# Kernel tuning notes

Hardware: AMD Instinct MI355X
Metric: run time of the kernel (lower is better)

## Reference

```python
import jax, jax.numpy as jnp
import numpy as np

D = 32       # d_model / hidden_size
H = 4        # n_heads
E = D // H   # head dim = 8
N = 2000     # nodes (hardcoded in FourierBlock weights / proj_class)
L = 96       # seq_len
MODES = (1, 4, 5)  # self.index hardcoded in FourierBlock
KAVG = 25    # moving_avg kernel (first of kernel list; layer uses res[0], trends[0])


def setup_inputs() -> dict:
    key = jax.random.key(0)
    ks = jax.random.split(key, 12)
    B = 8
    x = jax.random.normal(ks[0], (B, N, L, D), jnp.float32)
    lin = lambda k: jax.random.normal(k, (D, D), jnp.float32) * (1.0 / np.sqrt(D))
    scale = 1.0 / (D * D)  # FourierBlock: scale * torch.rand(...)
    W1 = jax.random.uniform(ks[5], (N, H, E, E, len(MODES)), jnp.float32) * scale
    W2 = jax.random.uniform(ks[6], (N, H, E, E, len(MODES)), jnp.float32) * scale
    return {
        "x": x,
        "Wq": lin(ks[1]), "bq": jnp.zeros((D,), jnp.float32),
        "Wk": lin(ks[2]), "bk": jnp.zeros((D,), jnp.float32),
        "Wv": lin(ks[3]), "bv": jnp.zeros((D,), jnp.float32),
        "Wo": lin(ks[4]), "bo": jnp.zeros((D,), jnp.float32),
        "W1": W1, "W2": W2,
    }


def _fourier_block(q, W1, W2):
    # q: [B, N, L, H, E] -> permute to [B, N, H, E, L] (torch: x = q.permute(0,1,3,4,2))
    B, Nn, Ll, Hh, Ee = q.shape
    xq = jnp.transpose(q, (0, 1, 3, 4, 2))
    x_ft = jnp.fft.rfft(xq, axis=-1)                 # [B, N, H, E, L//2+1] complex
    idx = jnp.array(MODES)
    xm = x_ft[..., idx]                              # [B, N, H, E, M]
    Wc = W1 + 1j * W2                                # complex per-node frequency weights
    out_m = jnp.einsum('bnhem,nheom->bnhom', xm, Wc.astype(jnp.complex64))
    F = Ll // 2 + 1
    out_ft = jnp.zeros((B, Nn, Hh, Ee, F), jnp.complex64).at[..., idx].set(out_m)
    y = jnp.fft.irfft(out_ft, n=Ll, axis=-1)         # [B, N, H, E, L]
    return jnp.transpose(y, (0, 1, 4, 2, 3))         # [B, N, L, H, E]


def _moving_avg(x, k):
    # replicate-pad the time axis by (k-1)//2 on each side, then mean over window k (stride 1)
    pad = (k - 1) // 2
    xp = jnp.pad(x, ((0, 0), (0, 0), (pad, pad), (0, 0)), mode='edge')
    cs = jnp.cumsum(xp, axis=2)
    cs = jnp.concatenate([jnp.zeros_like(cs[:, :, :1]), cs], axis=2)
    return (cs[:, :, k:] - cs[:, :, :-k]) / k        # [B, N, T, C]


def reference(x, Wq, bq, Wk, bk, Wv, bv, Wo, bo, W1, W2):
    B, Nn, Ll, Dm = x.shape
    # AutoCorrelationLayer projections
    q = (x @ Wq.T + bq).reshape(B, Nn, Ll, H, E)
    k = (x @ Wk.T + bk).reshape(B, Nn, Ll, H, E)   # faithful: computed, unused by FourierBlock
    v = (x @ Wv.T + bv).reshape(B, Nn, Ll, H, E)   # faithful: computed, unused by FourierBlock
    out = _fourier_block(q, W1, W2)                 # inner_correlation(q, k, v)
    out = out.reshape(B, Nn, Ll, Dm)
    new_x = out @ Wo.T + bo                         # out_projection
    # FFTDecompLayer: residual + series decomposition (eval mode, dropout=0)
    xr = x + new_x
    trend = _moving_avg(xr, KAVG)
    res = xr - trend
    return res
```

## Files before the change

### kernel.cpp

```cpp
#include <hip/hip_runtime.h>


#define N_NODES 2000

__global__ __launch_bounds__(256, 4)
void fused_fourier_decomp(const float* __restrict__ x,
                          const float* __restrict__ Wq,
                          const float* __restrict__ Wo,
                          const float* __restrict__ bo,
                          const float* __restrict__ W1,
                          const float* __restrict__ W2,
                          float* __restrict__ out)
{
  __shared__ __align__(16) float xT[32 * 97];
  __shared__ __align__(16) float basis[96 * 8];
  __shared__ __align__(16) float Wq_s[32 * 33];
  __shared__ __align__(16) float Wo_s[32 * 33];
  __shared__ __align__(16) float W1_s[768];
  __shared__ __align__(16) float W2_s[768];
  __shared__ __align__(16) float Z_s[32 * 8];
  __shared__ float bo_s[32];
  float* const pp = xT;
  float* const sbuf = xT + 1600;

  const int t = threadIdx.x;
  const int bid = blockIdx.x;
  const int n = bid % N_NODES;
  const size_t base = (size_t)bid * (96 * 32);

  const int d = t & 31;
  const int g = t >> 5;
  const int l0 = g * 12;

  float xv[12];
#pragma unroll
  for (int i = 0; i < 12; ++i)
    xv[i] = x[base + (size_t)(l0 + i) * 32 + d];

  for (int i = t; i < 1024; i += 256) {
    Wq_s[(i >> 5) * 33 + (i & 31)] = Wq[i];
    Wo_s[(i >> 5) * 33 + (i & 31)] = Wo[i];
  }
  {
    const float* W1p = W1 + n * 768;
    const float* W2p = W2 + n * 768;
    for (int i = t; i < 768; i += 256) {
      W1_s[i] = W1p[i];
      W2_s[i] = W2p[i];
    }
  }
  if (t < 32) bo_s[t] = bo[t];

  if (t < 96) {
    const int modes[3] = {1, 4, 5};
#pragma unroll
    for (int m = 0; m < 3; ++m) {
      int r = (modes[m] * t) % 96;
      float ang = (float)r * (6.28318530717958647692f / 96.0f);
      float sv, cv;
      sincosf(ang, &sv, &cv);
      basis[t * 8 + m] = cv;
      basis[t * 8 + 3 + m] = sv;
    }
    basis[t * 8 + 6] = 0.0f;
    basis[t * 8 + 7] = 0.0f;
  }
  __syncthreads();

  {
    float a0 = 0.f, a1 = 0.f, a2 = 0.f, a3 = 0.f, a4 = 0.f, a5 = 0.f;
#pragma unroll
    for (int i = 0; i < 12; ++i) {
      const int l = l0 + i;
      const float4 b0 = *(const float4*)&basis[l * 8];
      const float2 b1 = *(const float2*)&basis[l * 8 + 4];
      const float v = xv[i];
      a0 = fmaf(v, b0.x, a0);
      a1 = fmaf(v, b0.y, a1);
      a2 = fmaf(v, b0.z, a2);
      a3 = fmaf(v, b0.w, a3);
      a4 = fmaf(v, b1.x, a4);
      a5 = fmaf(v, b1.y, a5);
    }
    pp[g * 192 + 0 * 32 + d] = a0;
    pp[g * 192 + 1 * 32 + d] = a1;
    pp[g * 192 + 2 * 32 + d] = a2;
    pp[g * 192 + 3 * 32 + d] = a3;
    pp[g * 192 + 4 * 32 + d] = a4;
    pp[g * 192 + 5 * 32 + d] = a5;
  }
  __syncthreads();

  if (t < 64) {
    const int c = t & 31;
    const int jj = t >> 5;
    float* const csb = sbuf;
    float* const xsb = sbuf + 256;
    float* const osb = sbuf;

#pragma unroll
    for (int k = 0; k < 3; ++k) {
      const int j = jj * 3 + k;
      float s = 0.f;
#pragma unroll
      for (int gg = 0; gg < 8; ++gg) s += pp[gg * 192 + j * 32 + c];
      csb[c * 8 + j] = s;
    }
    __builtin_amdgcn_wave_barrier();

    {
      float X0 = 0.f, X1 = 0.f, X2 = 0.f;
#pragma unroll
      for (int dd = 0; dd < 32; ++dd) {
        const float w = Wq_s[c * 33 + dd];
        const int cb = dd * 8 + jj * 3;
        X0 = fmaf(w, csb[cb + 0], X0);
        X1 = fmaf(w, csb[cb + 1], X1);
        X2 = fmaf(w, csb[cb + 2], X2);
      }
      const float sgn = jj ? -1.f : 1.f;
      xsb[c * 8 + jj * 3 + 0] = sgn * X0;
      xsb[c * 8 + jj * 3 + 1] = sgn * X1;
      xsb[c * 8 + jj * 3 + 2] = sgn * X2;
    }
    __builtin_amdgcn_wave_barrier();

    {
      const int h = (t >> 3) & 3;
      const int o = t & 7;
      float od0 = 0.f, od1 = 0.f, od2 = 0.f;
#pragma unroll
      for (int e = 0; e < 8; ++e) {
        const int cp = h * 8 + e;
        const float4 xa = *(const float4*)&xsb[cp * 8];
        const float2 xb = *(const float2*)&xsb[cp * 8 + 4];
        const int wi = (cp * 8 + o) * 3;
        {
          const float w1 = W1_s[wi + 0], w2 = W2_s[wi + 0];
          const float a = jj ? w1 : -w2;
          const float b = jj ? w2 : w1;
          od0 = fmaf(xa.x, b, fmaf(xa.w, a, od0));
        }
        {
          const float w1 = W1_s[wi + 1], w2 = W2_s[wi + 1];
          const float a = jj ? w1 : -w2;
          const float b = jj ? w2 : w1;
          od1 = fmaf(xa.y, b, fmaf(xb.x, a, od1));
        }
        {
          const float w1 = W1_s[wi + 2], w2 = W2_s[wi + 2];
          const float a = jj ? w1 : -w2;
          const float b = jj ? w2 : w1;
          od2 = fmaf(xa.z, b, fmaf(xb.y, a, od2));
        }
      }
      const int cp = h * 8 + o;
      osb[cp * 8 + jj * 3 + 0] = od0;
      osb[cp * 8 + jj * 3 + 1] = od1;
      osb[cp * 8 + jj * 3 + 2] = od2;
    }
    __builtin_amdgcn_wave_barrier();

    {
      float z0 = 0.f, z1 = 0.f, z2 = 0.f;
#pragma unroll
      for (int cc = 0; cc < 32; ++cc) {
        const float w = Wo_s[c * 33 + cc];
        const int ob = cc * 8 + jj * 3;
        z0 = fmaf(w, osb[ob + 0], z0);
        z1 = fmaf(w, osb[ob + 1], z1);
        z2 = fmaf(w, osb[ob + 2], z2);
      }
      Z_s[c * 8 + jj * 3 + 0] = z0;
      Z_s[c * 8 + jj * 3 + 1] = z1;
      Z_s[c * 8 + jj * 3 + 2] = z2;
    }
  }
  __syncthreads();

  float xr[12];
  {
    const float4 z0 = *(const float4*)&Z_s[d * 8];
    const float2 z1 = *(const float2*)&Z_s[d * 8 + 4];
    const float bov = bo_s[d];
#pragma unroll
    for (int i = 0; i < 12; ++i) {
      const int l = l0 + i;
      const float4 b0 = *(const float4*)&basis[l * 8];
      const float2 b1 = *(const float2*)&basis[l * 8 + 4];
      const float v = z0.x * b0.x + z0.y * b0.y + z0.z * b0.z
                    - z0.w * b0.w - z1.x * b1.x - z1.y * b1.y;
      const float r = fmaf(v, (1.0f / 48.0f), bov) + xv[i];
      xr[i] = r;
      xT[d * 97 + l] = r;
    }
  }
  __syncthreads();

  {
    const float* col = &xT[d * 97];
    float lowv[12];
    float S = 0.f;
#pragma unroll
    for (int j = 0; j < 12; ++j) {
      int idx = l0 - 12 + j;
      idx = idx < 0 ? 0 : idx;
      lowv[j] = col[idx];
      S += lowv[j];
    }
#pragma unroll
    for (int i = 0; i < 12; ++i) S += xr[i];
    {
      int idx = l0 + 12;
      idx = idx > 95 ? 95 : idx;
      S += col[idx];
    }
#pragma unroll
    for (int i = 0; i < 12; ++i) {
      const int l = l0 + i;
      const float res = xr[i] - S * (1.0f / 25.0f);
      out[base + (size_t)l * 32 + d] = res;
      int hi = l + 13;
      hi = hi > 95 ? 95 : hi;
      S += col[hi] - lowv[i];
    }
  }
}

extern "C" void kernel_launch(void* const* d_in, const int* in_sizes, int n_in,
                              void* d_out, int out_size, void* d_ws, size_t ws_size,
                              hipStream_t stream) {
  (void)n_in; (void)out_size; (void)d_ws; (void)ws_size;
  const float* x  = (const float*)d_in[0];
  const float* Wq = (const float*)d_in[1];
  const float* Wo = (const float*)d_in[7];
  const float* bo = (const float*)d_in[8];
  const float* W1 = (const float*)d_in[9];
  const float* W2 = (const float*)d_in[10];
  float* out = (float*)d_out;

  const int blocks = in_sizes[0] / (96 * 32);
  fused_fourier_decomp<<<blocks, 256, 0, stream>>>(x, Wq, Wo, bo, W1, W2, out);
}
```

Measured before the change: 396.6 us.

## Process two same-node tiles per 512-thread block to share weight setup

Each block now handles two (batch, node) tiles that share the same node, using 512 threads. The per-block setup is loaded once and shared by both tiles: the Wq/Wo matrices, the per-node W1/W2 Fourier weights and the basis table. The per-node weights are aliased into the unused tail of the shared buffer to keep LDS usage down. The aim is to halve redundant setup traffic and shared-memory fills. It relies on half the tile count being a multiple of the node count (true for B=8), and the tighter launch bounds (512 threads, 8 blocks) may force register limits.

```diff
diff --git a/kernel.cpp b/kernel.cpp
--- a/kernel.cpp
+++ b/kernel.cpp
@@ -3,33 +3,39 @@
 
 #define N_NODES 2000
 
-__global__ __launch_bounds__(256, 4)
+__global__ __launch_bounds__(512, 8)
 void fused_fourier_decomp(const float* __restrict__ x,
                           const float* __restrict__ Wq,
                           const float* __restrict__ Wo,
                           const float* __restrict__ bo,
                           const float* __restrict__ W1,
                           const float* __restrict__ W2,
-                          float* __restrict__ out)
+                          float* __restrict__ out,
+                          const int halfTiles)
 {
-  __shared__ __align__(16) float xT[32 * 97];
+  __shared__ __align__(16) float xT[2 * 32 * 97];
   __shared__ __align__(16) float basis[96 * 8];
   __shared__ __align__(16) float Wq_s[32 * 33];
   __shared__ __align__(16) float Wo_s[32 * 33];
-  __shared__ __align__(16) float W1_s[768];
-  __shared__ __align__(16) float W2_s[768];
-  __shared__ __align__(16) float Z_s[32 * 8];
+  __shared__ __align__(16) float Z_s[2 * 32 * 8];
   __shared__ float bo_s[32];
-  float* const pp = xT;
-  float* const sbuf = xT + 1600;
-
-  const int t = threadIdx.x;
-  const int bid = blockIdx.x;
-  const int n = bid % N_NODES;
-  const size_t base = (size_t)bid * (96 * 32);
-
-  const int d = t & 31;
-  const int g = t >> 5;
+
+  const int t    = threadIdx.x;
+  const int tile = t >> 8;
+  const int tt   = t & 255;
+  const int n    = blockIdx.x % N_NODES;
+  const size_t bid  = (size_t)blockIdx.x + (size_t)tile * (size_t)halfTiles;
+  const size_t base = bid * (96 * 32);
+
+  float* const xTt  = xT + tile * 3104;
+  float* const pp   = xTt;
+  float* const sbuf = xTt + 1600;
+  float* const W1_s = xT + 2112;
+  float* const W2_s = xT + 3104 + 2112;
+  float* const Zt   = Z_s + tile * 256;
+
+  const int d  = tt & 31;
+  const int g  = tt >> 5;
   const int l0 = g * 12;
 
   float xv[12];
@@ -37,14 +43,14 @@
   for (int i = 0; i < 12; ++i)
     xv[i] = x[base + (size_t)(l0 + i) * 32 + d];
 
-  for (int i = t; i < 1024; i += 256) {
+  for (int i = t; i < 1024; i += 512) {
     Wq_s[(i >> 5) * 33 + (i & 31)] = Wq[i];
     Wo_s[(i >> 5) * 33 + (i & 31)] = Wo[i];
   }
   {
     const float* W1p = W1 + n * 768;
     const float* W2p = W2 + n * 768;
-    for (int i = t; i < 768; i += 256) {
+    for (int i = t; i < 768; i += 512) {
       W1_s[i] = W1p[i];
       W2_s[i] = W2p[i];
     }
@@ -91,9 +97,9 @@
   }
   __syncthreads();
 
-  if (t < 64) {
-    const int c = t & 31;
-    const int jj = t >> 5;
+  if (tt < 64) {
+    const int c  = tt & 31;
+    const int jj = tt >> 5;
     float* const csb = sbuf;
     float* const xsb = sbuf + 256;
     float* const osb = sbuf;
@@ -126,8 +132,8 @@
     __builtin_amdgcn_wave_barrier();
 
     {
-      const int h = (t >> 3) & 3;
-      const int o = t & 7;
+      const int h = (tt >> 3) & 3;
+      const int o = tt & 7;
       float od0 = 0.f, od1 = 0.f, od2 = 0.f;
 #pragma unroll
       for (int e = 0; e < 8; ++e) {
@@ -171,17 +177,17 @@
         z1 = fmaf(w, osb[ob + 1], z1);
         z2 = fmaf(w, osb[ob + 2], z2);
       }
-      Z_s[c * 8 + jj * 3 + 0] = z0;
-      Z_s[c * 8 + jj * 3 + 1] = z1;
-      Z_s[c * 8 + jj * 3 + 2] = z2;
+      Zt[c * 8 + jj * 3 + 0] = z0;
+      Zt[c * 8 + jj * 3 + 1] = z1;
+      Zt[c * 8 + jj * 3 + 2] = z2;
     }
   }
   __syncthreads();
 
   float xr[12];
   {
-    const float4 z0 = *(const float4*)&Z_s[d * 8];
-    const float2 z1 = *(const float2*)&Z_s[d * 8 + 4];
+    const float4 z0 = *(const float4*)&Zt[d * 8];
+    const float2 z1 = *(const float2*)&Zt[d * 8 + 4];
     const float bov = bo_s[d];
 #pragma unroll
     for (int i = 0; i < 12; ++i) {
@@ -192,13 +198,13 @@
                     - z0.w * b0.w - z1.x * b1.x - z1.y * b1.y;
       const float r = fmaf(v, (1.0f / 48.0f), bov) + xv[i];
       xr[i] = r;
-      xT[d * 97 + l] = r;
-    }
-  }
-  __syncthreads();
-
-  {
-    const float* col = &xT[d * 97];
+      xTt[d * 97 + l] = r;
+    }
+  }
+  __syncthreads();
+
+  {
+    const float* col = &xTt[d * 97];
     float lowv[12];
     float S = 0.f;
 #pragma unroll
@@ -239,6 +245,8 @@
   const float* W2 = (const float*)d_in[10];
   float* out = (float*)d_out;
 
-  const int blocks = in_sizes[0] / (96 * 32);
-  fused_fourier_decomp<<<blocks, 256, 0, stream>>>(x, Wq, Wo, bo, W1, W2, out);
+  const int tiles = in_sizes[0] / (96 * 32);
+  const int halfTiles = tiles / 2;
+  fused_fourier_decomp<<<halfTiles, 512, 0, stream>>>(x, Wq, Wo, bo, W1, W2, out,
+                                                      halfTiles);
 }
```

New measurement: 434.8 us. 9.6% more time.

## Drop Wq/Wo shared staging and repack spectral weights for vectorized LDS reads

Applied to the files above, without the earlier changes.

Wq and Wo are no longer staged in shared memory. Each thread reads its row straight from global into registers as float4. W1 and W2 are interleaved into one padded per-output-channel shared array, so the complex mode mix can read them with float4/float2 loads. The intermediate csb/xsb/osb buffers are transposed to mode-major order so the projections and reductions use vector LDS accesses. This cuts shared-memory footprint and LDS instruction count, but adds global (cache) loads in the 64-thread section and a scattered-index write when staging W1/W2.

```diff
diff --git a/kernel.cpp b/kernel.cpp
--- a/kernel.cpp
+++ b/kernel.cpp
@@ -14,14 +14,13 @@
 {
   __shared__ __align__(16) float xT[32 * 97];
   __shared__ __align__(16) float basis[96 * 8];
-  __shared__ __align__(16) float Wq_s[32 * 33];
-  __shared__ __align__(16) float Wo_s[32 * 33];
-  __shared__ __align__(16) float W1_s[768];
-  __shared__ __align__(16) float W2_s[768];
+  __shared__ __align__(16) float W12_s[32 * 68];
   __shared__ __align__(16) float Z_s[32 * 8];
   __shared__ float bo_s[32];
-  float* const pp = xT;
-  float* const sbuf = xT + 1600;
+  float* const pp  = xT;
+  float* const csb = xT + 1600;
+  float* const xsb = xT + 1792;
+  float* const osb = xT + 1600;
 
   const int t = threadIdx.x;
   const int bid = blockIdx.x;
@@ -37,16 +36,17 @@
   for (int i = 0; i < 12; ++i)
     xv[i] = x[base + (size_t)(l0 + i) * 32 + d];
 
-  for (int i = t; i < 1024; i += 256) {
-    Wq_s[(i >> 5) * 33 + (i & 31)] = Wq[i];
-    Wo_s[(i >> 5) * 33 + (i & 31)] = Wo[i];
-  }
-  {
-    const float* W1p = W1 + n * 768;
-    const float* W2p = W2 + n * 768;
+  {
+    const float* W1p = W1 + (size_t)n * 768;
+    const float* W2p = W2 + (size_t)n * 768;
     for (int i = t; i < 768; i += 256) {
-      W1_s[i] = W1p[i];
-      W2_s[i] = W2p[i];
+      const int m = i % 3;
+      const int o = (i / 3) & 7;
+      const int e = (i / 24) & 7;
+      const int h = i / 192;
+      const int dst = (h * 8 + o) * 68 + e * 8 + m;
+      W12_s[dst]     = W1p[i];
+      W12_s[dst + 3] = W2p[i];
     }
   }
   if (t < 32) bo_s[t] = bo[t];
@@ -92,88 +92,115 @@
   __syncthreads();
 
   if (t < 64) {
-    const int c = t & 31;
+    const int c  = t & 31;
     const int jj = t >> 5;
-    float* const csb = sbuf;
-    float* const xsb = sbuf + 256;
-    float* const osb = sbuf;
-
-#pragma unroll
-    for (int k = 0; k < 3; ++k) {
-      const int j = jj * 3 + k;
-      float s = 0.f;
-#pragma unroll
-      for (int gg = 0; gg < 8; ++gg) s += pp[gg * 192 + j * 32 + c];
-      csb[c * 8 + j] = s;
+
+    if (t < 48) {
+      const int j = t >> 3, cq = t & 7;
+      float4 acc = make_float4(0.f, 0.f, 0.f, 0.f);
+#pragma unroll
+      for (int gg = 0; gg < 8; ++gg) {
+        const float4 p = *(const float4*)&pp[gg * 192 + j * 32 + cq * 4];
+        acc.x += p.x; acc.y += p.y; acc.z += p.z; acc.w += p.w;
+      }
+      *(float4*)&csb[j * 32 + cq * 4] = acc;
     }
     __builtin_amdgcn_wave_barrier();
 
     {
+      const float* wqr = Wq + c * 32;
+      float4 wq4[8];
+#pragma unroll
+      for (int q = 0; q < 8; ++q) wq4[q] = *(const float4*)&wqr[q * 4];
+      const int jb = jj * 3;
       float X0 = 0.f, X1 = 0.f, X2 = 0.f;
 #pragma unroll
-      for (int dd = 0; dd < 32; ++dd) {
-        const float w = Wq_s[c * 33 + dd];
-        const int cb = dd * 8 + jj * 3;
-        X0 = fmaf(w, csb[cb + 0], X0);
-        X1 = fmaf(w, csb[cb + 1], X1);
-        X2 = fmaf(w, csb[cb + 2], X2);
+      for (int q = 0; q < 8; ++q) {
+        const float4 w  = wq4[q];
+        const float4 c0 = *(const float4*)&csb[(jb + 0) * 32 + q * 4];
+        const float4 c1 = *(const float4*)&csb[(jb + 1) * 32 + q * 4];
+        const float4 c2 = *(const float4*)&csb[(jb + 2) * 32 + q * 4];
+        X0 = fmaf(w.x, c0.x, X0); X0 = fmaf(w.y, c0.y, X0);
+        X0 = fmaf(w.z, c0.z, X0); X0 = fmaf(w.w, c0.w, X0);
+        X1 = fmaf(w.x, c1.x, X1); X1 = fmaf(w.y, c1.y, X1);
+        X1 = fmaf(w.z, c1.z, X1); X1 = fmaf(w.w, c1.w, X1);
+        X2 = fmaf(w.x, c2.x, X2); X2 = fmaf(w.y, c2.y, X2);
+        X2 = fmaf(w.z, c2.z, X2); X2 = fmaf(w.w, c2.w, X2);
       }
       const float sgn = jj ? -1.f : 1.f;
-      xsb[c * 8 + jj * 3 + 0] = sgn * X0;
-      xsb[c * 8 + jj * 3 + 1] = sgn * X1;
-      xsb[c * 8 + jj * 3 + 2] = sgn * X2;
+      xsb[(jb + 0) * 32 + c] = sgn * X0;
+      xsb[(jb + 1) * 32 + c] = sgn * X1;
+      xsb[(jb + 2) * 32 + c] = sgn * X2;
     }
     __builtin_amdgcn_wave_barrier();
 
     {
       const int h = (t >> 3) & 3;
       const int o = t & 7;
+      const int cp = h * 8 + o;
+      const float* wrow = &W12_s[cp * 68];
       float od0 = 0.f, od1 = 0.f, od2 = 0.f;
-#pragma unroll
-      for (int e = 0; e < 8; ++e) {
-        const int cp = h * 8 + e;
-        const float4 xa = *(const float4*)&xsb[cp * 8];
-        const float2 xb = *(const float2*)&xsb[cp * 8 + 4];
-        const int wi = (cp * 8 + o) * 3;
-        {
-          const float w1 = W1_s[wi + 0], w2 = W2_s[wi + 0];
-          const float a = jj ? w1 : -w2;
-          const float b = jj ? w2 : w1;
-          od0 = fmaf(xa.x, b, fmaf(xa.w, a, od0));
-        }
-        {
-          const float w1 = W1_s[wi + 1], w2 = W2_s[wi + 1];
-          const float a = jj ? w1 : -w2;
-          const float b = jj ? w2 : w1;
-          od1 = fmaf(xa.y, b, fmaf(xb.x, a, od1));
-        }
-        {
-          const float w1 = W1_s[wi + 2], w2 = W2_s[wi + 2];
-          const float a = jj ? w1 : -w2;
-          const float b = jj ? w2 : w1;
-          od2 = fmaf(xa.z, b, fmaf(xb.y, a, od2));
-        }
-      }
-      const int cp = h * 8 + o;
-      osb[cp * 8 + jj * 3 + 0] = od0;
-      osb[cp * 8 + jj * 3 + 1] = od1;
-      osb[cp * 8 + jj * 3 + 2] = od2;
+
+#define DSTEP(XC, E_) do {                                                  \
+        const float4 wa = *(const float4*)&wrow[(E_) * 8];      \
+        const float2 wb = *(const float2*)&wrow[(E_) * 8 + 4];     \
+        { const float a = jj ? wa.x : -wa.w; const float b = jj ? wa.w : wa.x;    \
+          od0 = fmaf(xr0.XC, b, fmaf(xi0.XC, a, od0)); }                          \
+        { const float a = jj ? wa.y : -wb.x; const float b = jj ? wb.x : wa.y;    \
+          od1 = fmaf(xr1.XC, b, fmaf(xi1.XC, a, od1)); }                          \
+        { const float a = jj ? wa.z : -wb.y; const float b = jj ? wb.y : wa.z;    \
+          od2 = fmaf(xr2.XC, b, fmaf(xi2.XC, a, od2)); }                          \
+      } while (0)
+
+      {
+        const float4 xr0 = *(const float4*)&xsb[0 * 32 + h * 8];
+        const float4 xr1 = *(const float4*)&xsb[1 * 32 + h * 8];
+        const float4 xr2 = *(const float4*)&xsb[2 * 32 + h * 8];
+        const float4 xi0 = *(const float4*)&xsb[3 * 32 + h * 8];
+        const float4 xi1 = *(const float4*)&xsb[4 * 32 + h * 8];
+        const float4 xi2 = *(const float4*)&xsb[5 * 32 + h * 8];
+        DSTEP(x, 0); DSTEP(y, 1); DSTEP(z, 2); DSTEP(w, 3);
+      }
+      {
+        const float4 xr0 = *(const float4*)&xsb[0 * 32 + h * 8 + 4];
+        const float4 xr1 = *(const float4*)&xsb[1 * 32 + h * 8 + 4];
+        const float4 xr2 = *(const float4*)&xsb[2 * 32 + h * 8 + 4];
+        const float4 xi0 = *(const float4*)&xsb[3 * 32 + h * 8 + 4];
+        const float4 xi1 = *(const float4*)&xsb[4 * 32 + h * 8 + 4];
+        const float4 xi2 = *(const float4*)&xsb[5 * 32 + h * 8 + 4];
+        DSTEP(x, 4); DSTEP(y, 5); DSTEP(z, 6); DSTEP(w, 7);
+      }
+#undef DSTEP
+
+      osb[(jj * 3 + 0) * 32 + cp] = od0;
+      osb[(jj * 3 + 1) * 32 + cp] = od1;
+      osb[(jj * 3 + 2) * 32 + cp] = od2;
     }
     __builtin_amdgcn_wave_barrier();
 
     {
-      float z0 = 0.f, z1 = 0.f, z2 = 0.f;
-#pragma unroll
-      for (int cc = 0; cc < 32; ++cc) {
-        const float w = Wo_s[c * 33 + cc];
-        const int ob = cc * 8 + jj * 3;
-        z0 = fmaf(w, osb[ob + 0], z0);
-        z1 = fmaf(w, osb[ob + 1], z1);
-        z2 = fmaf(w, osb[ob + 2], z2);
-      }
-      Z_s[c * 8 + jj * 3 + 0] = z0;
-      Z_s[c * 8 + jj * 3 + 1] = z1;
-      Z_s[c * 8 + jj * 3 + 2] = z2;
+      const float* wor = Wo + c * 32;
+      float4 wo4[8];
+#pragma unroll
+      for (int q = 0; q < 8; ++q) wo4[q] = *(const float4*)&wor[q * 4];
+      const int jb = jj * 3;
+      float Z0 = 0.f, Z1 = 0.f, Z2 = 0.f;
+#pragma unroll
+      for (int q = 0; q < 8; ++q) {
+        const float4 w  = wo4[q];
+        const float4 o0 = *(const float4*)&osb[(jb + 0) * 32 + q * 4];
+        const float4 o1 = *(const float4*)&osb[(jb + 1) * 32 + q * 4];
+        const float4 o2 = *(const float4*)&osb[(jb + 2) * 32 + q * 4];
+        Z0 = fmaf(w.x, o0.x, Z0); Z0 = fmaf(w.y, o0.y, Z0);
+        Z0 = fmaf(w.z, o0.z, Z0); Z0 = fmaf(w.w, o0.w, Z0);
+        Z1 = fmaf(w.x, o1.x, Z1); Z1 = fmaf(w.y, o1.y, Z1);
+        Z1 = fmaf(w.z, o1.z, Z1); Z1 = fmaf(w.w, o1.w, Z1);
+        Z2 = fmaf(w.x, o2.x, Z2); Z2 = fmaf(w.y, o2.y, Z2);
+        Z2 = fmaf(w.z, o2.z, Z2); Z2 = fmaf(w.w, o2.w, Z2);
+      }
+      Z_s[c * 8 + jb + 0] = Z0;
+      Z_s[c * 8 + jb + 1] = Z1;
+      Z_s[c * 8 + jb + 2] = Z2;
     }
   }
   __syncthreads();
```

After: 387.5 us. 1.02x faster.
